# Optimization experiments

Hardware: AMD Instinct MI355X
Metric: run time of the kernel (lower is better)

Reference implementation:

```python
import jax, jax.numpy as jnp
import numpy as np

HEAD = 8
PAD = (2, 2)   # (mod//2, mod//2 + mod%2) for dim=508, head=8 -> mod=4
EPS = 1e-6


def setup_inputs() -> dict:
    key = jax.random.key(0)
    ks = jax.random.split(key, 4)
    d_pad = 512  # 508 + mod(4)
    s = 1.0 / np.sqrt(d_pad).astype(np.float32)
    inp = jax.random.normal(ks[0], (2, 2048, 508), dtype=jnp.float32)
    Wq = jax.random.normal(ks[1], (d_pad, d_pad), dtype=jnp.float32) * s
    Wk = jax.random.normal(ks[2], (d_pad, d_pad), dtype=jnp.float32) * s
    Wv = jax.random.normal(ks[3], (d_pad, d_pad), dtype=jnp.float32) * s
    gamma = jnp.ones((d_pad,), dtype=jnp.float32)
    beta = jnp.zeros((d_pad,), dtype=jnp.float32)
    return {"inp": inp, "Wq": Wq, "Wk": Wk, "Wv": Wv, "gamma": gamma, "beta": beta}


def reference(inp, Wq, Wk, Wv, gamma, beta):
    # pad feature dim so it divides head count (torch F.pad on last dim)
    x = jnp.pad(inp, ((0, 0), (0, 0), (PAD[0], PAD[1])))  # [B, L, D]
    residual = x
    b, l, d = x.shape
    h = HEAD
    dh = d // h
    inv_sqrt_dh = 1.0 / np.sqrt(dh).astype(np.float32)

    def proj(W):
        # torch Linear (no bias): x @ W.T ; then split heads -> [B, H, L, dh]
        return (x @ W.T).reshape(b, l, h, dh).transpose(0, 2, 1, 3)

    q = proj(Wq)
    k = proj(Wk)
    v = proj(Wv)

    score = jnp.einsum('bhld,bhmd->bhlm', q, k) * inv_sqrt_dh  # [B,H,L,L]
    attn = jax.nn.softmax(score, axis=-1)
    out = jnp.einsum('bhlm,bhmd->bhld', attn, v)               # [B,H,L,dh]
    out = out.transpose(0, 2, 1, 3).reshape(b, l, d)           # unshape

    # dropout is identity in eval mode; residual + layernorm
    y = out + residual
    mu = jnp.mean(y, axis=-1, keepdims=True)
    var = jnp.mean(jnp.square(y - mu), axis=-1, keepdims=True)
    z = (y - mu) / jnp.sqrt(var + EPS)
    out = gamma * z + beta

    out = out[:, :, PAD[0]:-PAD[1]]  # strip padding back to original dim
    return out, attn
```

## Files before the change

kernel.cpp:

```cpp
#include <hip/hip_runtime.h>

typedef short bf16x8 __attribute__((ext_vector_type(8)));
typedef float f32x4 __attribute__((ext_vector_type(4)));
typedef unsigned short u16;
typedef u16 u16x8 __attribute__((ext_vector_type(8)));
typedef u16 u16x4 __attribute__((ext_vector_type(4)));

#define L_ 2048
#define D_ 512
#define H_ 8
#define DH_ 64
#define DIN 508

static __device__ __forceinline__ u16 f2b(float f){
  unsigned u = __builtin_bit_cast(unsigned, f);
  unsigned r = u + 0x7fffu + ((u >> 16) & 1u);
  return (u16)(r >> 16);
}
static __device__ __forceinline__ float b2f(u16 u){
  unsigned x = ((unsigned)u) << 16;
  return __builtin_bit_cast(float, x);
}
static __device__ __forceinline__ bf16x8 asbf(u16x8 v){
  return __builtin_bit_cast(bf16x8, v);
}
#define MFMA16(a,b,c) __builtin_amdgcn_mfma_f32_16x16x32_bf16(a,b,c,0,0,0)

__global__ __launch_bounds__(512) void cvt_kernel(
    const float* __restrict__ inp, const float* __restrict__ Wq,
    const float* __restrict__ Wk, const float* __restrict__ Wv,
    u16* __restrict__ Xb, u16* __restrict__ Wb)
{
  const int tid = blockIdx.x*512 + threadIdx.x;
  if (tid < 262144) {
    const int idx8 = tid*8;
    const int row = idx8 >> 9, col = idx8 & 511;
    u16x8 o;
    #pragma unroll
    for (int e=0;e<8;++e){
      const int c = col+e;
      const float v = (c>=2 && c<510) ? inp[(size_t)row*DIN + (c-2)] : 0.f;
      o[e] = f2b(v);
    }
    *(u16x8*)&Xb[idx8] = o;
  } else {
    const int idx8 = (tid - 262144)*8;
    const int row = idx8 >> 9, col = idx8 & 511;
    const float* __restrict__ W = (row < 512) ? Wq : (row < 1024) ? Wk : Wv;
    const float* p = &W[(size_t)(row & 511)*D_ + col];
    u16x8 o;
    #pragma unroll
    for (int e=0;e<8;++e) o[e] = f2b(p[e]);
    *(u16x8*)&Wb[idx8] = o;
  }
}

__global__ __launch_bounds__(512) void proj_kernel(
    const u16* __restrict__ Xb, const u16* __restrict__ Wb,
    u16* __restrict__ Qg, u16* __restrict__ Kg, u16* __restrict__ Vt)
{
  __shared__ u16 Xl[128*72];
  __shared__ u16 Wl[128*72];
  const int t = threadIdx.x;
  const int lane = t & 63, wid = t >> 6;
  const int wr = wid >> 2, wc = wid & 3;
  const int i0 = blockIdx.x * 128;
  const int j0 = blockIdx.y * 128;
  const int mat = j0 >> 9;
  const int srow = t >> 3, sc8 = (t & 7) * 8;

  f32x4 acc[4][2];
  #pragma unroll
  for (int a=0;a<4;++a){
    #pragma unroll
    for (int bq=0;bq<2;++bq){ f32x4 z = {0.f,0.f,0.f,0.f}; acc[a][bq] = z; }
  }

  u16x8 xa0 = *(const u16x8*)&Xb[(size_t)(i0+srow)*D_ + sc8];
  u16x8 xa1 = *(const u16x8*)&Xb[(size_t)(i0+64+srow)*D_ + sc8];
  u16x8 wa0 = *(const u16x8*)&Wb[(size_t)(j0+srow)*D_ + sc8];
  u16x8 wa1 = *(const u16x8*)&Wb[(size_t)(j0+64+srow)*D_ + sc8];

  for (int kt=0; kt<8; ++kt){
    __syncthreads();
    *(u16x8*)&Xl[srow*72 + sc8] = xa0;
    *(u16x8*)&Xl[(64+srow)*72 + sc8] = xa1;
    *(u16x8*)&Wl[srow*72 + sc8] = wa0;
    *(u16x8*)&Wl[(64+srow)*72 + sc8] = wa1;
    __syncthreads();
    if (kt < 7){
      const int k1 = (kt+1)*64;
      xa0 = *(const u16x8*)&Xb[(size_t)(i0+srow)*D_ + k1 + sc8];
      xa1 = *(const u16x8*)&Xb[(size_t)(i0+64+srow)*D_ + k1 + sc8];
      wa0 = *(const u16x8*)&Wb[(size_t)(j0+srow)*D_ + k1 + sc8];
      wa1 = *(const u16x8*)&Wb[(size_t)(j0+64+srow)*D_ + k1 + sc8];
    }
    #pragma unroll
    for (int ks=0; ks<2; ++ks){
      const int ko = ks*32 + (lane>>4)*8;
      bf16x8 af[4], bfr[2];
      #pragma unroll
      for (int fm=0; fm<4; ++fm)
        af[fm] = *(const bf16x8*)&Xl[(wr*64 + fm*16 + (lane&15))*72 + ko];
      #pragma unroll
      for (int fn=0; fn<2; ++fn)
        bfr[fn] = *(const bf16x8*)&Wl[(wc*32 + fn*16 + (lane&15))*72 + ko];
      #pragma unroll
      for (int fm=0; fm<4; ++fm){
        #pragma unroll
        for (int fn=0; fn<2; ++fn)
          acc[fm][fn] = MFMA16(af[fm], bfr[fn], acc[fm][fn]);
      }
    }
  }
  #pragma unroll
  for (int fm=0; fm<4; ++fm){
    const int ibase = i0 + wr*64 + fm*16 + (lane>>4)*4;
    const int b = ibase >> 11;
    const int li = ibase & (L_-1);
    #pragma unroll
    for (int fn=0; fn<2; ++fn){
      const int n = j0 + wc*32 + fn*16 + (lane&15);
      const int h = (n>>6) & 7;
      const int dh = n & 63;
      if (mat == 2){
        u16x4 pk;
        #pragma unroll
        for (int r=0;r<4;++r) pk[r] = f2b(acc[fm][fn][r]);
        *(u16x4*)&Vt[((size_t)(b*H_+h)*DH_ + dh)*L_ + li] = pk;
      } else {
        u16* dst = ((mat==0)? Qg : Kg) + ((size_t)(b*H_+h)*L_ + li)*DH_ + dh;
        #pragma unroll
        for (int r=0;r<4;++r) dst[(size_t)r*DH_] = f2b(acc[fm][fn][r]);
      }
    }
  }
}

__global__ __launch_bounds__(512, 4) void attn_kernel(
    const u16* __restrict__ Qg, const u16* __restrict__ Kg,
    const u16* __restrict__ Vt, float* __restrict__ attn, float* __restrict__ Og)
{
  __shared__ u16 Kl[128*72];
  __shared__ u16 Vl[64*136];
  __shared__ u16 Pt[32*136];
  __shared__ float rsp[8][32];
  __shared__ float inv_rs[32];

  const int t = threadIdx.x, lane = t & 63, wid = t >> 6;
  const int q0 = blockIdx.x * 32;
  const int bh = blockIdx.y;
  const u16* Qp = Qg + ((size_t)bh*L_ + q0)*DH_;
  const u16* Kp = Kg + (size_t)bh*L_*DH_;
  const u16* Vp = Vt + (size_t)bh*DH_*L_;

  bf16x8 qf[2][2];
  #pragma unroll
  for (int qi=0;qi<2;++qi){
    #pragma unroll
    for (int ks=0;ks<2;++ks)
      qf[qi][ks] = *(const bf16x8*)&Qp[(size_t)(qi*16 + (lane&15))*DH_ + ks*32 + (lane>>4)*8];
  }

  const int kr0 = t>>3, kc8 = (t&7)*8;
  const int vr0 = t>>4, vcm = (t&15)*8;
  const int g4 = (lane>>4)*8;
  const int mrow = wid*16 + (lane&15);

  float racc0 = 0.f, racc1 = 0.f;
  u16x8 ka = *(const u16x8*)&Kp[(size_t)kr0*DH_ + kc8];
  u16x8 kb = *(const u16x8*)&Kp[(size_t)(64+kr0)*DH_ + kc8];
  for (int kt=0; kt<16; ++kt){
    __syncthreads();
    *(u16x8*)&Kl[kr0*72 + kc8] = ka;
    *(u16x8*)&Kl[(64+kr0)*72 + kc8] = kb;
    __syncthreads();
    if (kt < 15){
      ka = *(const u16x8*)&Kp[(size_t)((kt+1)*128 + kr0)*DH_ + kc8];
      kb = *(const u16x8*)&Kp[(size_t)((kt+1)*128 + 64 + kr0)*DH_ + kc8];
    }
    bf16x8 kf0 = *(const bf16x8*)&Kl[mrow*72 + g4];
    bf16x8 kf1 = *(const bf16x8*)&Kl[mrow*72 + 32 + g4];
    f32x4 s0 = {0.f,0.f,0.f,0.f}, s1 = {0.f,0.f,0.f,0.f};
    s0 = MFMA16(kf0, qf[0][0], s0); s0 = MFMA16(kf1, qf[0][1], s0);
    s1 = MFMA16(kf0, qf[1][0], s1); s1 = MFMA16(kf1, qf[1][1], s1);
    #pragma unroll
    for (int r=0;r<4;++r){
      racc0 += __expf(s0[r]*0.125f);
      racc1 += __expf(s1[r]*0.125f);
    }
  }
  racc0 += __shfl_xor(racc0, 16); racc0 += __shfl_xor(racc0, 32);
  racc1 += __shfl_xor(racc1, 16); racc1 += __shfl_xor(racc1, 32);
  if (lane < 16){ rsp[wid][lane] = racc0; rsp[wid][16+lane] = racc1; }
  __syncthreads();
  if (t < 32){
    float s = 0.f;
    #pragma unroll
    for (int w=0;w<8;++w) s += rsp[w][t];
    inv_rs[t] = 1.f/s;
  }
  __syncthreads();

  const int qpv = wid>>2, d0 = (wid&3)*16;
  f32x4 o0 = {0.f,0.f,0.f,0.f}, o1 = {0.f,0.f,0.f,0.f};
  const int sr = t >> 4;
  const int sc = (t & 15) * 8;
  float* abase = attn + ((size_t)bh*L_ + q0 + sr)*L_ + sc;

  ka = *(const u16x8*)&Kp[(size_t)kr0*DH_ + kc8];
  kb = *(const u16x8*)&Kp[(size_t)(64+kr0)*DH_ + kc8];
  u16x8 va = *(const u16x8*)&Vp[(size_t)vr0*L_ + vcm];
  u16x8 vb = *(const u16x8*)&Vp[(size_t)(32+vr0)*L_ + vcm];
  for (int kt=0; kt<16; ++kt){
    __syncthreads();
    *(u16x8*)&Kl[kr0*72 + kc8] = ka;
    *(u16x8*)&Kl[(64+kr0)*72 + kc8] = kb;
    *(u16x8*)&Vl[vr0*136 + vcm] = va;
    *(u16x8*)&Vl[(32+vr0)*136 + vcm] = vb;
    __syncthreads();
    if (kt < 15){
      ka = *(const u16x8*)&Kp[(size_t)((kt+1)*128 + kr0)*DH_ + kc8];
      kb = *(const u16x8*)&Kp[(size_t)((kt+1)*128 + 64 + kr0)*DH_ + kc8];
      va = *(const u16x8*)&Vp[(size_t)vr0*L_ + (kt+1)*128 + vcm];
      vb = *(const u16x8*)&Vp[(size_t)(32+vr0)*L_ + (kt+1)*128 + vcm];
    }
    bf16x8 kf0 = *(const bf16x8*)&Kl[mrow*72 + g4];
    bf16x8 kf1 = *(const bf16x8*)&Kl[mrow*72 + 32 + g4];
    f32x4 s0 = {0.f,0.f,0.f,0.f}, s1 = {0.f,0.f,0.f,0.f};
    s0 = MFMA16(kf0, qf[0][0], s0); s0 = MFMA16(kf1, qf[0][1], s0);
    s1 = MFMA16(kf0, qf[1][0], s1); s1 = MFMA16(kf1, qf[1][1], s1);
    u16x4 p0, p1;
    p0[0] = f2b(__expf(s0[0]*0.125f)); p0[1] = f2b(__expf(s0[1]*0.125f));
    p0[2] = f2b(__expf(s0[2]*0.125f)); p0[3] = f2b(__expf(s0[3]*0.125f));
    p1[0] = f2b(__expf(s1[0]*0.125f)); p1[1] = f2b(__expf(s1[1]*0.125f));
    p1[2] = f2b(__expf(s1[2]*0.125f)); p1[3] = f2b(__expf(s1[3]*0.125f));
    *(u16x4*)&Pt[(lane&15)*136 + wid*16 + (lane>>4)*4] = p0;
    *(u16x4*)&Pt[(16 + (lane&15))*136 + wid*16 + (lane>>4)*4] = p1;
    __syncthreads();
    {
      const u16x8 pv8 = *(const u16x8*)&Pt[sr*136 + sc];
      const float inv = inv_rs[sr];
      f32x4 w0, w1;
      w0[0]=b2f(pv8[0])*inv; w0[1]=b2f(pv8[1])*inv;
      w0[2]=b2f(pv8[2])*inv; w0[3]=b2f(pv8[3])*inv;
      w1[0]=b2f(pv8[4])*inv; w1[1]=b2f(pv8[5])*inv;
      w1[2]=b2f(pv8[6])*inv; w1[3]=b2f(pv8[7])*inv;
      __builtin_nontemporal_store(w0, (f32x4*)&abase[kt*128]);
      __builtin_nontemporal_store(w1, (f32x4*)&abase[kt*128 + 4]);
    }
    #pragma unroll
    for (int ms=0; ms<4; ++ms){
      bf16x8 pa = *(const bf16x8*)&Pt[(qpv*16 + (lane&15))*136 + ms*32 + g4];
      bf16x8 vv = *(const bf16x8*)&Vl[(d0 + (lane&15))*136 + ms*32 + g4];
      if (ms&1) o1 = MFMA16(pa, vv, o1); else o0 = MFMA16(pa, vv, o0);
    }
  }
  {
    const int b = bh>>3, h = bh&7;
    #pragma unroll
    for (int r=0;r<4;++r){
      const int qr = qpv*16 + (lane>>4)*4 + r;
      Og[((size_t)(b*L_ + q0 + qr))*D_ + h*DH_ + d0 + (lane&15)] = (o0[r]+o1[r])*inv_rs[qr];
    }
  }
}

__global__ __launch_bounds__(256) void ln_kernel(
    const float* __restrict__ Og, const float* __restrict__ inp,
    const float* __restrict__ gamma, const float* __restrict__ beta,
    float* __restrict__ out0)
{
  const int row = blockIdx.x, t = threadIdx.x;
  const int lane = t & 63, wid = t >> 6;
  const int c2 = t + 256;
  const float x1 = (t >= 2) ? inp[(size_t)row*DIN + t-2] : 0.f;
  const float x2 = (c2 < 510) ? inp[(size_t)row*DIN + c2-2] : 0.f;
  const float y1 = Og[(size_t)row*D_ + t]  + x1;
  const float y2 = Og[(size_t)row*D_ + c2] + x2;
  float s = y1 + y2, ss = y1*y1 + y2*y2;
  #pragma unroll
  for (int off=1; off<64; off<<=1){
    s  += __shfl_xor(s,  off);
    ss += __shfl_xor(ss, off);
  }
  __shared__ float red[4][2];
  if (lane == 0){ red[wid][0] = s; red[wid][1] = ss; }
  __syncthreads();
  s  = red[0][0]+red[1][0]+red[2][0]+red[3][0];
  ss = red[0][1]+red[1][1]+red[2][1]+red[3][1];
  const float mu   = s * (1.f/512.f);
  const float var  = ss * (1.f/512.f) - mu*mu;
  const float rstd = rsqrtf(var + 1e-6f);
  const float z1 = (y1 - mu)*rstd*gamma[t]  + beta[t];
  const float z2 = (y2 - mu)*rstd*gamma[c2] + beta[c2];
  if (t >= 2)   out0[(size_t)row*DIN + t-2]  = z1;
  if (c2 < 510) out0[(size_t)row*DIN + c2-2] = z2;
}

extern "C" void kernel_launch(void* const* d_in, const int* in_sizes, int n_in,
                              void* d_out, int out_size, void* d_ws, size_t ws_size,
                              hipStream_t stream) {
  const float* inp   = (const float*)d_in[0];
  const float* Wq    = (const float*)d_in[1];
  const float* Wk    = (const float*)d_in[2];
  const float* Wv    = (const float*)d_in[3];
  const float* gamma = (const float*)d_in[4];
  const float* beta  = (const float*)d_in[5];

  char* ws = (char*)d_ws;
  u16*   Qg = (u16*)(ws);
  u16*   Kg = (u16*)(ws + 4194304);
  u16*   Vt = (u16*)(ws + 8388608);
  float* Og = (float*)(ws + 12582912);
  u16*   Xb = (u16*)(ws + 12582912);
  u16*   Wb = (u16*)(ws + 16777216);

  float* out0 = (float*)d_out;
  float* attn = out0 + 2080768;

  cvt_kernel <<<704, 512, 0, stream>>>(inp, Wq, Wk, Wv, Xb, Wb);
  proj_kernel<<<dim3(32,12), 512, 0, stream>>>(Xb, Wb, Qg, Kg, Vt);
  attn_kernel<<<dim3(64,16), 512, 0, stream>>>(Qg, Kg, Vt, attn, Og);
  ln_kernel  <<<4096, 256, 0, stream>>>(Og, inp, gamma, beta, out0);
}
```

Baseline: 126.1 us.

## Load K fragments directly to registers and double-buffer P/V with one barrier per tile

```diff
diff --git a/kernel.cpp b/kernel.cpp
--- a/kernel.cpp
+++ b/kernel.cpp
@@ -11,6 +11,7 @@
 #define H_ 8
 #define DH_ 64
 #define DIN 508
+#define EXPC 0.18033688011112042f
 
 static __device__ __forceinline__ u16 f2b(float f){
   unsigned u = __builtin_bit_cast(unsigned, f);
@@ -141,9 +142,8 @@
     const u16* __restrict__ Qg, const u16* __restrict__ Kg,
     const u16* __restrict__ Vt, float* __restrict__ attn, float* __restrict__ Og)
 {
-  __shared__ u16 Kl[128*72];
-  __shared__ u16 Vl[64*136];
-  __shared__ u16 Pt[32*136];
+  __shared__ u16 Vbuf[2][64*140];
+  __shared__ u16 Pbuf[2][32*136];
   __shared__ float rsp[8][32];
   __shared__ float inv_rs[32];
 
@@ -162,32 +162,28 @@
       qf[qi][ks] = *(const bf16x8*)&Qp[(size_t)(qi*16 + (lane&15))*DH_ + ks*32 + (lane>>4)*8];
   }
 
-  const int kr0 = t>>3, kc8 = (t&7)*8;
   const int vr0 = t>>4, vcm = (t&15)*8;
   const int g4 = (lane>>4)*8;
   const int mrow = wid*16 + (lane&15);
 
   float racc0 = 0.f, racc1 = 0.f;
-  u16x8 ka = *(const u16x8*)&Kp[(size_t)kr0*DH_ + kc8];
-  u16x8 kb = *(const u16x8*)&Kp[(size_t)(64+kr0)*DH_ + kc8];
-  for (int kt=0; kt<16; ++kt){
-    __syncthreads();
-    *(u16x8*)&Kl[kr0*72 + kc8] = ka;
-    *(u16x8*)&Kl[(64+kr0)*72 + kc8] = kb;
-    __syncthreads();
-    if (kt < 15){
-      ka = *(const u16x8*)&Kp[(size_t)((kt+1)*128 + kr0)*DH_ + kc8];
-      kb = *(const u16x8*)&Kp[(size_t)((kt+1)*128 + 64 + kr0)*DH_ + kc8];
-    }
-    bf16x8 kf0 = *(const bf16x8*)&Kl[mrow*72 + g4];
-    bf16x8 kf1 = *(const bf16x8*)&Kl[mrow*72 + 32 + g4];
-    f32x4 s0 = {0.f,0.f,0.f,0.f}, s1 = {0.f,0.f,0.f,0.f};
-    s0 = MFMA16(kf0, qf[0][0], s0); s0 = MFMA16(kf1, qf[0][1], s0);
-    s1 = MFMA16(kf0, qf[1][0], s1); s1 = MFMA16(kf1, qf[1][1], s1);
-    #pragma unroll
-    for (int r=0;r<4;++r){
-      racc0 += __expf(s0[r]*0.125f);
-      racc1 += __expf(s1[r]*0.125f);
+  {
+    u16x8 nk0 = *(const u16x8*)&Kp[(size_t)mrow*DH_ + g4];
+    u16x8 nk1 = *(const u16x8*)&Kp[(size_t)mrow*DH_ + 32 + g4];
+    for (int kt=0; kt<16; ++kt){
+      bf16x8 kf0 = asbf(nk0), kf1 = asbf(nk1);
+      if (kt < 15){
+        nk0 = *(const u16x8*)&Kp[(size_t)((kt+1)*128 + mrow)*DH_ + g4];
+        nk1 = *(const u16x8*)&Kp[(size_t)((kt+1)*128 + mrow)*DH_ + 32 + g4];
+      }
+      f32x4 s0 = {0.f,0.f,0.f,0.f}, s1 = {0.f,0.f,0.f,0.f};
+      s0 = MFMA16(kf0, qf[0][0], s0); s0 = MFMA16(kf1, qf[0][1], s0);
+      s1 = MFMA16(kf0, qf[1][0], s1); s1 = MFMA16(kf1, qf[1][1], s1);
+      #pragma unroll
+      for (int r=0;r<4;++r){
+        racc0 += exp2f(s0[r]*EXPC);
+        racc1 += exp2f(s1[r]*EXPC);
+      }
     }
   }
   racc0 += __shfl_xor(racc0, 16); racc0 += __shfl_xor(racc0, 32);
@@ -207,54 +203,64 @@
   const int sr = t >> 4;
   const int sc = (t & 15) * 8;
   float* abase = attn + ((size_t)bh*L_ + q0 + sr)*L_ + sc;
-
-  ka = *(const u16x8*)&Kp[(size_t)kr0*DH_ + kc8];
-  kb = *(const u16x8*)&Kp[(size_t)(64+kr0)*DH_ + kc8];
-  u16x8 va = *(const u16x8*)&Vp[(size_t)vr0*L_ + vcm];
-  u16x8 vb = *(const u16x8*)&Vp[(size_t)(32+vr0)*L_ + vcm];
+  const float sinv = inv_rs[sr];
+
+  {
+    u16x8 k0 = *(const u16x8*)&Kp[(size_t)mrow*DH_ + g4];
+    u16x8 k1 = *(const u16x8*)&Kp[(size_t)mrow*DH_ + 32 + g4];
+    u16x8 va = *(const u16x8*)&Vp[(size_t)vr0*L_ + vcm];
+    u16x8 vb = *(const u16x8*)&Vp[(size_t)(32+vr0)*L_ + vcm];
+    f32x4 s0 = {0.f,0.f,0.f,0.f}, s1 = {0.f,0.f,0.f,0.f};
+    s0 = MFMA16(asbf(k0), qf[0][0], s0); s0 = MFMA16(asbf(k1), qf[0][1], s0);
+    s1 = MFMA16(asbf(k0), qf[1][0], s1); s1 = MFMA16(asbf(k1), qf[1][1], s1);
+    u16x4 p0, p1;
+    #pragma unroll
+    for (int r=0;r<4;++r){ p0[r] = f2b(exp2f(s0[r]*EXPC)); p1[r] = f2b(exp2f(s1[r]*EXPC)); }
+    *(u16x4*)&Pbuf[0][(lane&15)*136 + wid*16 + (lane>>4)*4] = p0;
+    *(u16x4*)&Pbuf[0][(16 + (lane&15))*136 + wid*16 + (lane>>4)*4] = p1;
+    *(u16x8*)&Vbuf[0][vr0*140 + vcm] = va;
+    *(u16x8*)&Vbuf[0][(32+vr0)*140 + vcm] = vb;
+  }
+  __syncthreads();
+
   for (int kt=0; kt<16; ++kt){
-    __syncthreads();
-    *(u16x8*)&Kl[kr0*72 + kc8] = ka;
-    *(u16x8*)&Kl[(64+kr0)*72 + kc8] = kb;
-    *(u16x8*)&Vl[vr0*136 + vcm] = va;
-    *(u16x8*)&Vl[(32+vr0)*136 + vcm] = vb;
-    __syncthreads();
+    const int cur = kt & 1;
+    u16x8 k0, k1, va, vb;
     if (kt < 15){
-      ka = *(const u16x8*)&Kp[(size_t)((kt+1)*128 + kr0)*DH_ + kc8];
-      kb = *(const u16x8*)&Kp[(size_t)((kt+1)*128 + 64 + kr0)*DH_ + kc8];
+      k0 = *(const u16x8*)&Kp[(size_t)((kt+1)*128 + mrow)*DH_ + g4];
+      k1 = *(const u16x8*)&Kp[(size_t)((kt+1)*128 + mrow)*DH_ + 32 + g4];
       va = *(const u16x8*)&Vp[(size_t)vr0*L_ + (kt+1)*128 + vcm];
       vb = *(const u16x8*)&Vp[(size_t)(32+vr0)*L_ + (kt+1)*128 + vcm];
     }
-    bf16x8 kf0 = *(const bf16x8*)&Kl[mrow*72 + g4];
-    bf16x8 kf1 = *(const bf16x8*)&Kl[mrow*72 + 32 + g4];
-    f32x4 s0 = {0.f,0.f,0.f,0.f}, s1 = {0.f,0.f,0.f,0.f};
-    s0 = MFMA16(kf0, qf[0][0], s0); s0 = MFMA16(kf1, qf[0][1], s0);
-    s1 = MFMA16(kf0, qf[1][0], s1); s1 = MFMA16(kf1, qf[1][1], s1);
-    u16x4 p0, p1;
-    p0[0] = f2b(__expf(s0[0]*0.125f)); p0[1] = f2b(__expf(s0[1]*0.125f));
-    p0[2] = f2b(__expf(s0[2]*0.125f)); p0[3] = f2b(__expf(s0[3]*0.125f));
-    p1[0] = f2b(__expf(s1[0]*0.125f)); p1[1] = f2b(__expf(s1[1]*0.125f));
-    p1[2] = f2b(__expf(s1[2]*0.125f)); p1[3] = f2b(__expf(s1[3]*0.125f));
-    *(u16x4*)&Pt[(lane&15)*136 + wid*16 + (lane>>4)*4] = p0;
-    *(u16x4*)&Pt[(16 + (lane&15))*136 + wid*16 + (lane>>4)*4] = p1;
-    __syncthreads();
     {
-      const u16x8 pv8 = *(const u16x8*)&Pt[sr*136 + sc];
-      const float inv = inv_rs[sr];
+      const u16x8 pv8 = *(const u16x8*)&Pbuf[cur][sr*136 + sc];
       f32x4 w0, w1;
-      w0[0]=b2f(pv8[0])*inv; w0[1]=b2f(pv8[1])*inv;
-      w0[2]=b2f(pv8[2])*inv; w0[3]=b2f(pv8[3])*inv;
-      w1[0]=b2f(pv8[4])*inv; w1[1]=b2f(pv8[5])*inv;
-      w1[2]=b2f(pv8[6])*inv; w1[3]=b2f(pv8[7])*inv;
+      w0[0]=b2f(pv8[0])*sinv; w0[1]=b2f(pv8[1])*sinv;
+      w0[2]=b2f(pv8[2])*sinv; w0[3]=b2f(pv8[3])*sinv;
+      w1[0]=b2f(pv8[4])*sinv; w1[1]=b2f(pv8[5])*sinv;
+      w1[2]=b2f(pv8[6])*sinv; w1[3]=b2f(pv8[7])*sinv;
       __builtin_nontemporal_store(w0, (f32x4*)&abase[kt*128]);
       __builtin_nontemporal_store(w1, (f32x4*)&abase[kt*128 + 4]);
     }
     #pragma unroll
     for (int ms=0; ms<4; ++ms){
-      bf16x8 pa = *(const bf16x8*)&Pt[(qpv*16 + (lane&15))*136 + ms*32 + g4];
-      bf16x8 vv = *(const bf16x8*)&Vl[(d0 + (lane&15))*136 + ms*32 + g4];
+      bf16x8 pa = *(const bf16x8*)&Pbuf[cur][(qpv*16 + (lane&15))*136 + ms*32 + g4];
+      bf16x8 vv = *(const bf16x8*)&Vbuf[cur][(d0 + (lane&15))*140 + ms*32 + g4];
       if (ms&1) o1 = MFMA16(pa, vv, o1); else o0 = MFMA16(pa, vv, o0);
     }
+    if (kt < 15){
+      f32x4 s0 = {0.f,0.f,0.f,0.f}, s1 = {0.f,0.f,0.f,0.f};
+      s0 = MFMA16(asbf(k0), qf[0][0], s0); s0 = MFMA16(asbf(k1), qf[0][1], s0);
+      s1 = MFMA16(asbf(k0), qf[1][0], s1); s1 = MFMA16(asbf(k1), qf[1][1], s1);
+      u16x4 p0, p1;
+      #pragma unroll
+      for (int r=0;r<4;++r){ p0[r] = f2b(exp2f(s0[r]*EXPC)); p1[r] = f2b(exp2f(s1[r]*EXPC)); }
+      *(u16x4*)&Pbuf[cur^1][(lane&15)*136 + wid*16 + (lane>>4)*4] = p0;
+      *(u16x4*)&Pbuf[cur^1][(16 + (lane&15))*136 + wid*16 + (lane>>4)*4] = p1;
+      *(u16x8*)&Vbuf[cur^1][vr0*140 + vcm] = va;
+      *(u16x8*)&Vbuf[cur^1][(32+vr0)*140 + vcm] = vb;
+    }
+    __syncthreads();
   }
   {
     const int b = bh>>3, h = bh&7;
```

Result: slower. 189.4 us (+50.2%).
